# Kernel tuning notes

Measured on AMD Instinct MI355X. Metric: run time of the kernel, lower is better.

## Reference

```python
import jax, jax.numpy as jnp
import numpy as np

B, S, D, H = 2, 2048, 1024, 16
DK = D // H  # 64


def setup_inputs() -> dict:
    key = jax.random.key(0)
    ks = jax.random.split(key, 12)
    def lin(kw, kb, fan_in, shape_w):
        bound = 1.0 / np.sqrt(fan_in)
        W = jax.random.uniform(kw, shape_w, jnp.float32, -bound, bound)
        b = jax.random.uniform(kb, (shape_w[0],), jnp.float32, -bound, bound)
        return W, b
    Q = jax.random.normal(ks[0], (B, S, D), jnp.float32)
    K = jax.random.normal(ks[1], (B, S, D), jnp.float32)
    V = jax.random.normal(ks[2], (B, S, D), jnp.float32)
    attn_mask = jax.random.randint(ks[3], (B, S, S), 0, 2) == 1  # bool, True=masked
    Wq, bq = lin(ks[4], ks[5], D, (D, D))
    Wk, bk = lin(ks[6], ks[7], D, (D, D))
    Wv, bv = lin(ks[8], ks[9], D, (D, D))
    Wo, bo = lin(ks[10], ks[11], D, (D, D))
    return {"Q": Q, "K": K, "V": V, "attn_mask": attn_mask,
            "Wq": Wq, "bq": bq, "Wk": Wk, "bk": bk,
            "Wv": Wv, "bv": bv, "Wo": Wo, "bo": bo}


def reference(Q, K, V, attn_mask, Wq, bq, Wk, bk, Wv, bv, Wo, bo):
    b, s, d = Q.shape
    # project and split heads: [B,S,D] -> [B,H,S,DK]
    def heads(x, W, bias):
        y = x @ W.T + bias
        return y.reshape(b, -1, H, DK).transpose(0, 2, 1, 3)
    q = heads(Q, Wq, bq)
    k = heads(K, Wk, bk)
    v = heads(V, Wv, bv)
    # scaled dot-product attention with custom reweighting
    scores = jnp.einsum('bhqd,bhkd->bhqk', q, k) / np.sqrt(DK).astype(jnp.float32)
    scores = jnp.where(attn_mask[:, None, :, :], jnp.float32(-1e9), scores)
    attn_weights = jax.nn.softmax(scores, axis=-1) * scores.shape[-1]  # non-standard *S_k scale
    ctx = jnp.einsum('bhqk,bhkd->bhqd', attn_weights, v)
    ctx = ctx.transpose(0, 2, 1, 3).reshape(b, -1, H * DK)
    output = ctx @ Wo.T + bo
    return output, attn_weights
```

## Files before the change

kernel.cpp:

```cpp
#include <hip/hip_runtime.h>
#include <hip/hip_bf16.h>
#include <type_traits>

typedef __bf16 bf16_t;
typedef __attribute__((ext_vector_type(8))) __bf16 bf16x8;
typedef __attribute__((ext_vector_type(4))) float f32x4;

#define B_ 2
#define S_ 2048
#define D_ 1024
#define H_ 16
#define DK_ 64

__device__ inline void split8(const float* __restrict__ p, bf16x8& h, bf16x8& l) {
    float4 x0 = *(const float4*)p;
    float4 x1 = *(const float4*)(p + 4);
    float xs[8] = {x0.x, x0.y, x0.z, x0.w, x1.x, x1.y, x1.z, x1.w};
#pragma unroll
    for (int i = 0; i < 8; ++i) {
        bf16_t hh = (bf16_t)xs[i];
        h[i] = hh;
        l[i] = (bf16_t)(xs[i] - (float)hh);
    }
}
__device__ inline void hi8(const float* __restrict__ p, bf16x8& h) {
    float4 x0 = *(const float4*)p;
    float4 x1 = *(const float4*)(p + 4);
    float xs[8] = {x0.x, x0.y, x0.z, x0.w, x1.x, x1.y, x1.z, x1.w};
#pragma unroll
    for (int i = 0; i < 8; ++i) h[i] = (bf16_t)xs[i];
}

template <typename AT, typename OT, bool SPLIT>
__global__ __launch_bounds__(256) void gemm_bt(
    const AT* __restrict__ A,
    const float* __restrict__ W,
    const float* __restrict__ bias,
    OT* __restrict__ Y,
    int M, int N, int K)
{
    const int NB = N >> 6;
    const int bm = blockIdx.x / NB;
    const int bn = blockIdx.x % NB;
    const int tid  = threadIdx.x;
    const int wave = tid >> 6;
    const int lane = tid & 63;
    const int l16  = lane & 15;
    const int quad = lane >> 4;
    const int wm = wave >> 1, wn = wave & 1;

    __shared__ bf16_t Ah[64][40];
    __shared__ bf16_t Wh[64][40];
    __shared__ bf16_t Al[SPLIT ? 64 : 1][40];
    __shared__ bf16_t Wl[SPLIT ? 64 : 1][40];

    const int srow = tid >> 2;
    const int scol = (tid & 3) * 8;

    f32x4 acc[2][2];
#pragma unroll
    for (int i = 0; i < 2; ++i)
#pragma unroll
        for (int j = 0; j < 2; ++j) acc[i][j] = (f32x4){0.f, 0.f, 0.f, 0.f};

    const AT*    Arow = A + (size_t)(bm * 64 + srow) * K + scol;
    const float* Wrow = W + (size_t)(bn * 64 + srow) * K + scol;

    for (int k0 = 0; k0 < K; k0 += 32) {
        if constexpr (std::is_same_v<AT, float>) {
            bf16x8 ah, al;
            if constexpr (SPLIT) {
                split8(Arow + k0, ah, al);
                *(bf16x8*)(&Al[srow][scol]) = al;
            } else {
                hi8(Arow + k0, ah);
            }
            *(bf16x8*)(&Ah[srow][scol]) = ah;
        } else {
            *(bf16x8*)(&Ah[srow][scol]) = *(const bf16x8*)(Arow + k0);
        }
        {
            bf16x8 wh, wl;
            if constexpr (SPLIT) {
                split8(Wrow + k0, wh, wl);
                *(bf16x8*)(&Wl[srow][scol]) = wl;
            } else {
                hi8(Wrow + k0, wh);
            }
            *(bf16x8*)(&Wh[srow][scol]) = wh;
        }
        __syncthreads();

        bf16x8 afh[2], bfh[2], afl[2], bfl[2];
#pragma unroll
        for (int mi = 0; mi < 2; ++mi) {
            afh[mi] = *(const bf16x8*)(&Ah[wm * 32 + mi * 16 + l16][quad * 8]);
            if constexpr (SPLIT)
                afl[mi] = *(const bf16x8*)(&Al[wm * 32 + mi * 16 + l16][quad * 8]);
        }
#pragma unroll
        for (int ni = 0; ni < 2; ++ni) {
            bfh[ni] = *(const bf16x8*)(&Wh[wn * 32 + ni * 16 + l16][quad * 8]);
            if constexpr (SPLIT)
                bfl[ni] = *(const bf16x8*)(&Wl[wn * 32 + ni * 16 + l16][quad * 8]);
        }

#pragma unroll
        for (int mi = 0; mi < 2; ++mi)
#pragma unroll
            for (int ni = 0; ni < 2; ++ni) {
                acc[mi][ni] = __builtin_amdgcn_mfma_f32_16x16x32_bf16(
                    afh[mi], bfh[ni], acc[mi][ni], 0, 0, 0);
                if constexpr (SPLIT) {
                    acc[mi][ni] = __builtin_amdgcn_mfma_f32_16x16x32_bf16(
                        afl[mi], bfh[ni], acc[mi][ni], 0, 0, 0);
                    acc[mi][ni] = __builtin_amdgcn_mfma_f32_16x16x32_bf16(
                        afh[mi], bfl[ni], acc[mi][ni], 0, 0, 0);
                }
            }
        __syncthreads();
    }

#pragma unroll
    for (int ni = 0; ni < 2; ++ni) {
        const int col = bn * 64 + wn * 32 + ni * 16 + l16;
        const float bv = bias[col];
#pragma unroll
        for (int mi = 0; mi < 2; ++mi) {
#pragma unroll
            for (int r = 0; r < 4; ++r) {
                const int row = bm * 64 + wm * 32 + mi * 16 + quad * 4 + r;
                Y[(size_t)row * N + col] = (OT)(acc[mi][ni][r] + bv);
            }
        }
    }
}

__global__ __launch_bounds__(256) void pack_mask(
    const int* __restrict__ mask,
    unsigned long long* __restrict__ pk)
{
    const size_t nwords = (size_t)B_ * S_ * S_ / 64;
    const int lane = threadIdx.x & 63;
    size_t w = (size_t)blockIdx.x * 4 + (threadIdx.x >> 6);
    const size_t stride = (size_t)gridDim.x * 4;
    for (; w < nwords; w += stride) {
        const int m = mask[w * 64 + lane];
        const unsigned long long bb = __ballot(m != 0);
        if (lane == 0) pk[w] = bb;
    }
}

__global__ __launch_bounds__(256) void attn_kernel(
    const float*  __restrict__ qp,
    const float*  __restrict__ kp,
    const bf16_t* __restrict__ vp,
    const unsigned* __restrict__ pm,
    float* __restrict__ wout,
    float* __restrict__ normbuf,
    bf16_t* __restrict__ ctx)
{
    const int bid = blockIdx.x;
    const int qt = bid & 31;
    const int h  = (bid >> 5) & 15;
    const int b  = bid >> 9;
    const int tid  = threadIdx.x;
    const int wave = tid >> 6;
    const int lane = tid & 63;
    const int l16  = lane & 15;
    const int quad = lane >> 4;

    const int q0 = qt * 64 + wave * 16;

    __shared__ bf16_t Kh[32][72];
    __shared__ bf16_t Kl[32][72];
    __shared__ bf16_t vT[64][40];
    __shared__ bf16_t wl[4][16][40];

    const float* qbase = qp + ((size_t)(b * S_ + q0 + l16)) * D_ + h * DK_ + quad * 8;
    bf16x8 qh0, ql0, qh1, ql1;
    split8(qbase, qh0, ql0);
    split8(qbase + 32, qh1, ql1);

    const float scale = 0.125f;

    const int srow = tid >> 3;
    const int scol = (tid & 7) * 8;
    const float*  kst = kp + (size_t)b * S_ * D_ + h * DK_;
    const bf16_t* vst = vp + (size_t)b * S_ * D_ + h * DK_;

    const unsigned* pmrow = pm + (size_t)b * S_ * (S_ / 32);
    const size_t wbase = ((size_t)(b * H_ + h)) * S_ * S_;

    float lsum[4] = {0.f, 0.f, 0.f, 0.f};
    f32x4 acc[4];
#pragma unroll
    for (int t = 0; t < 4; ++t) acc[t] = (f32x4){0.f, 0.f, 0.f, 0.f};

    for (int j0 = 0; j0 < S_; j0 += 32) {
        {
            bf16x8 kh, kl;
            split8(kst + (size_t)(j0 + srow) * D_ + scol, kh, kl);
            *(bf16x8*)(&Kh[srow][scol]) = kh;
            *(bf16x8*)(&Kl[srow][scol]) = kl;

            const bf16x8 vv = *(const bf16x8*)(vst + (size_t)(j0 + srow) * D_ + scol);
#pragma unroll
            for (int i = 0; i < 8; ++i) vT[scol + i][srow] = vv[i];
        }
        unsigned mw[4];
#pragma unroll
        for (int r = 0; r < 4; ++r) {
            const int q = q0 + quad * 4 + r;
            mw[r] = pmrow[(size_t)q * (S_ / 32) + (j0 >> 5)];
        }
        __syncthreads();

#pragma unroll
        for (int sub = 0; sub < 2; ++sub) {
            const int rr = sub * 16 + l16;
            const bf16x8 kh0 = *(const bf16x8*)(&Kh[rr][quad * 8]);
            const bf16x8 kh1 = *(const bf16x8*)(&Kh[rr][32 + quad * 8]);
            const bf16x8 kl0 = *(const bf16x8*)(&Kl[rr][quad * 8]);
            const bf16x8 kl1 = *(const bf16x8*)(&Kl[rr][32 + quad * 8]);
            f32x4 c = (f32x4){0.f, 0.f, 0.f, 0.f};
            c = __builtin_amdgcn_mfma_f32_16x16x32_bf16(qh0, kh0, c, 0, 0, 0);
            c = __builtin_amdgcn_mfma_f32_16x16x32_bf16(qh1, kh1, c, 0, 0, 0);
            c = __builtin_amdgcn_mfma_f32_16x16x32_bf16(ql0, kh0, c, 0, 0, 0);
            c = __builtin_amdgcn_mfma_f32_16x16x32_bf16(ql1, kh1, c, 0, 0, 0);
            c = __builtin_amdgcn_mfma_f32_16x16x32_bf16(qh0, kl0, c, 0, 0, 0);
            c = __builtin_amdgcn_mfma_f32_16x16x32_bf16(qh1, kl1, c, 0, 0, 0);
            const int jt = j0 + sub * 16;
#pragma unroll
            for (int r = 0; r < 4; ++r) {
                const int q = q0 + quad * 4 + r;
                const int msk = (mw[r] >> (sub * 16 + l16)) & 1;
                const float e = msk ? 0.f : __expf(c[r] * scale);
                lsum[r] += e;
                __builtin_nontemporal_store(e, &wout[wbase + (size_t)q * S_ + jt + l16]);
                wl[wave][quad * 4 + r][sub * 16 + l16] = (bf16_t)e;
            }
        }
        const bf16x8 wa = *(const bf16x8*)(&wl[wave][l16][quad * 8]);
#pragma unroll
        for (int t = 0; t < 4; ++t) {
            const bf16x8 vf = *(const bf16x8*)(&vT[t * 16 + l16][quad * 8]);
            acc[t] = __builtin_amdgcn_mfma_f32_16x16x32_bf16(wa, vf, acc[t], 0, 0, 0);
        }
        __syncthreads();
    }

#pragma unroll
    for (int r = 0; r < 4; ++r) {
        float v = lsum[r];
        v += __shfl_xor(v, 1);
        v += __shfl_xor(v, 2);
        v += __shfl_xor(v, 4);
        v += __shfl_xor(v, 8);
        lsum[r] = v;
    }
    float norm[4];
#pragma unroll
    for (int r = 0; r < 4; ++r) norm[r] = 2048.f / lsum[r];

    if (l16 == 0) {
#pragma unroll
        for (int r = 0; r < 4; ++r)
            normbuf[(size_t)(b * H_ + h) * S_ + q0 + quad * 4 + r] = norm[r];
    }

#pragma unroll
    for (int t = 0; t < 4; ++t) {
#pragma unroll
        for (int r = 0; r < 4; ++r) {
            const int q = q0 + quad * 4 + r;
            ctx[((size_t)(b * S_ + q)) * D_ + h * DK_ + t * 16 + l16] =
                (bf16_t)(acc[t][r] * norm[r]);
        }
    }
}

__global__ __launch_bounds__(256) void rescale_wout(
    float* __restrict__ wout,
    const float* __restrict__ normbuf)
{
    const size_t total = (size_t)B_ * H_ * S_ * (S_ / 4);
    f32x4* wp = (f32x4*)wout;
    for (size_t i = (size_t)blockIdx.x * blockDim.x + threadIdx.x;
         i < total;
         i += (size_t)gridDim.x * blockDim.x) {
        const float n = normbuf[i >> 9];
        f32x4 w = __builtin_nontemporal_load(wp + i);
        w *= n;
        __builtin_nontemporal_store(w, wp + i);
    }
}

extern "C" void kernel_launch(void* const* d_in, const int* in_sizes, int n_in,
                              void* d_out, int out_size, void* d_ws, size_t ws_size,
                              hipStream_t stream) {
    const float* Q    = (const float*)d_in[0];
    const float* K    = (const float*)d_in[1];
    const float* V    = (const float*)d_in[2];
    const int*   mask = (const int*)d_in[3];
    const float* Wq   = (const float*)d_in[4];
    const float* bq   = (const float*)d_in[5];
    const float* Wk   = (const float*)d_in[6];
    const float* bk   = (const float*)d_in[7];
    const float* Wv   = (const float*)d_in[8];
    const float* bv   = (const float*)d_in[9];
    const float* Wo   = (const float*)d_in[10];
    const float* bo   = (const float*)d_in[11];

    const size_t BSD = (size_t)B_ * S_ * D_;
    float* out  = (float*)d_out;
    float* wout = out + BSD;

    float*  qp  = (float*)d_ws;
    float*  kpf = qp + BSD;
    bf16_t* vp  = (bf16_t*)(kpf + BSD);
    bf16_t* cx  = vp + BSD;
    unsigned long long* pk = (unsigned long long*)(cx + BSD);
    float* normbuf = (float*)((unsigned*)pk + (size_t)B_ * S_ * (S_ / 32));

    const int M = B_ * S_;
    const int N = D_;
    const int Kd = D_;
    const dim3 ggrid((M / 64) * (N / 64));
    const dim3 gblk(256);

    pack_mask<<<dim3(512), gblk, 0, stream>>>(mask, pk);

    gemm_bt<float, float, true><<<ggrid, gblk, 0, stream>>>(Q, Wq, bq, qp, M, N, Kd);
    gemm_bt<float, float, true><<<ggrid, gblk, 0, stream>>>(K, Wk, bk, kpf, M, N, Kd);
    gemm_bt<float, bf16_t, false><<<ggrid, gblk, 0, stream>>>(V, Wv, bv, vp, M, N, Kd);

    attn_kernel<<<dim3(B_ * H_ * (S_ / 64)), gblk, 0, stream>>>(
        qp, kpf, vp, (const unsigned*)pk, wout, normbuf, cx);

    gemm_bt<bf16_t, float, false><<<ggrid, gblk, 0, stream>>>(cx, Wo, bo, out, M, N, Kd);

    rescale_wout<<<dim3(2048), gblk, 0, stream>>>(wout, normbuf);
}
```

Measured before the change: 1.071 ms.

## Emit pre-split bf16 Q/K and head-transposed V from projection GEMMs

The projection GEMM epilogues now write Q and K as separate bf16 hi/lo planes, and V as bf16 in a per-head transposed [B,H,DK,S] layout. The attention kernel loads these directly instead of re-splitting fp32 K on every tile and transposing V element by element into shared memory. This cuts global read bytes for K and removes redundant conversion and scattered LDS writes in the hot loop. The cost is that the V epilogue now does strided scattered 2-byte global writes, and the Q/K GEMMs write two outputs each.

```diff
diff --git a/kernel.cpp b/kernel.cpp
--- a/kernel.cpp
+++ b/kernel.cpp
@@ -12,6 +12,8 @@
 #define H_ 16
 #define DK_ 64
 
+enum { OM_F32 = 0, OM_BF16 = 1, OM_SPLIT = 2, OM_HEADT = 3 };
+
 __device__ inline void split8(const float* __restrict__ p, bf16x8& h, bf16x8& l) {
     float4 x0 = *(const float4*)p;
     float4 x1 = *(const float4*)(p + 4);
@@ -31,12 +33,13 @@
     for (int i = 0; i < 8; ++i) h[i] = (bf16_t)xs[i];
 }
 
-template <typename AT, typename OT, bool SPLIT>
+template <typename AT, int OMODE, bool SPLIT>
 __global__ __launch_bounds__(256) void gemm_bt(
     const AT* __restrict__ A,
     const float* __restrict__ W,
     const float* __restrict__ bias,
-    OT* __restrict__ Y,
+    void* __restrict__ Yp,
+    void* __restrict__ Y2p,
     int M, int N, int K)
 {
     const int NB = N >> 6;
@@ -130,7 +133,23 @@
 #pragma unroll
             for (int r = 0; r < 4; ++r) {
                 const int row = bm * 64 + wm * 32 + mi * 16 + quad * 4 + r;
-                Y[(size_t)row * N + col] = (OT)(acc[mi][ni][r] + bv);
+                const float v = acc[mi][ni][r] + bv;
+                if constexpr (OMODE == OM_F32) {
+                    ((float*)Yp)[(size_t)row * N + col] = v;
+                } else if constexpr (OMODE == OM_BF16) {
+                    ((bf16_t*)Yp)[(size_t)row * N + col] = (bf16_t)v;
+                } else if constexpr (OMODE == OM_SPLIT) {
+                    const bf16_t hh = (bf16_t)v;
+                    ((bf16_t*)Yp)[(size_t)row * N + col] = hh;
+                    ((bf16_t*)Y2p)[(size_t)row * N + col] = (bf16_t)(v - (float)hh);
+                } else {
+                    const int bb  = row >> 11;
+                    const int ss  = row & (S_ - 1);
+                    const int hh2 = col >> 6;
+                    const int dk  = col & (DK_ - 1);
+                    ((bf16_t*)Yp)[((size_t)((bb * H_ + hh2) * DK_ + dk) << 11) + ss] =
+                        (bf16_t)v;
+                }
             }
         }
     }
@@ -152,9 +171,11 @@
 }
 
 __global__ __launch_bounds__(256) void attn_kernel(
-    const float*  __restrict__ qp,
-    const float*  __restrict__ kp,
-    const bf16_t* __restrict__ vp,
+    const bf16_t* __restrict__ qh_g,
+    const bf16_t* __restrict__ ql_g,
+    const bf16_t* __restrict__ kh_g,
+    const bf16_t* __restrict__ kl_g,
+    const bf16_t* __restrict__ vt_g,
     const unsigned* __restrict__ pm,
     float* __restrict__ wout,
     float* __restrict__ normbuf,
@@ -177,17 +198,21 @@
     __shared__ bf16_t vT[64][40];
     __shared__ bf16_t wl[4][16][40];
 
-    const float* qbase = qp + ((size_t)(b * S_ + q0 + l16)) * D_ + h * DK_ + quad * 8;
-    bf16x8 qh0, ql0, qh1, ql1;
-    split8(qbase, qh0, ql0);
-    split8(qbase + 32, qh1, ql1);
+    const size_t qoff = ((size_t)(b * S_ + q0 + l16)) * D_ + h * DK_ + quad * 8;
+    const bf16x8 qh0 = *(const bf16x8*)(qh_g + qoff);
+    const bf16x8 qh1 = *(const bf16x8*)(qh_g + qoff + 32);
+    const bf16x8 ql0 = *(const bf16x8*)(ql_g + qoff);
+    const bf16x8 ql1 = *(const bf16x8*)(ql_g + qoff + 32);
 
     const float scale = 0.125f;
 
-    const int srow = tid >> 3;
-    const int scol = (tid & 7) * 8;
-    const float*  kst = kp + (size_t)b * S_ * D_ + h * DK_;
-    const bf16_t* vst = vp + (size_t)b * S_ * D_ + h * DK_;
+    const int srow  = tid >> 3;
+    const int scol  = (tid & 7) * 8;
+    const int srow2 = tid >> 2;
+    const int scol2 = (tid & 3) * 8;
+    const bf16_t* khst = kh_g + (size_t)b * S_ * D_ + h * DK_;
+    const bf16_t* klst = kl_g + (size_t)b * S_ * D_ + h * DK_;
+    const bf16_t* vtst = vt_g + ((size_t)(b * H_ + h) * DK_ + srow2) * S_ + scol2;
 
     const unsigned* pmrow = pm + (size_t)b * S_ * (S_ / 32);
     const size_t wbase = ((size_t)(b * H_ + h)) * S_ * S_;
@@ -199,14 +224,10 @@
 
     for (int j0 = 0; j0 < S_; j0 += 32) {
         {
-            bf16x8 kh, kl;
-            split8(kst + (size_t)(j0 + srow) * D_ + scol, kh, kl);
-            *(bf16x8*)(&Kh[srow][scol]) = kh;
-            *(bf16x8*)(&Kl[srow][scol]) = kl;
-
-            const bf16x8 vv = *(const bf16x8*)(vst + (size_t)(j0 + srow) * D_ + scol);
-#pragma unroll
-            for (int i = 0; i < 8; ++i) vT[scol + i][srow] = vv[i];
+            const size_t ko = (size_t)(j0 + srow) * D_ + scol;
+            *(bf16x8*)(&Kh[srow][scol]) = *(const bf16x8*)(khst + ko);
+            *(bf16x8*)(&Kl[srow][scol]) = *(const bf16x8*)(klst + ko);
+            *(bf16x8*)(&vT[srow2][scol2]) = *(const bf16x8*)(vtst + j0);
         }
         unsigned mw[4];
 #pragma unroll
@@ -316,10 +337,12 @@
     float* out  = (float*)d_out;
     float* wout = out + BSD;
 
-    float*  qp  = (float*)d_ws;
-    float*  kpf = qp + BSD;
-    bf16_t* vp  = (bf16_t*)(kpf + BSD);
-    bf16_t* cx  = vp + BSD;
+    bf16_t* qh = (bf16_t*)d_ws;
+    bf16_t* ql = qh + BSD;
+    bf16_t* kh = ql + BSD;
+    bf16_t* kl = kh + BSD;
+    bf16_t* vt = kl + BSD;
+    bf16_t* cx = vt + BSD;
     unsigned long long* pk = (unsigned long long*)(cx + BSD);
     float* normbuf = (float*)((unsigned*)pk + (size_t)B_ * S_ * (S_ / 32));
 
@@ -331,14 +354,14 @@
 
     pack_mask<<<dim3(512), gblk, 0, stream>>>(mask, pk);
 
-    gemm_bt<float, float, true><<<ggrid, gblk, 0, stream>>>(Q, Wq, bq, qp, M, N, Kd);
-    gemm_bt<float, float, true><<<ggrid, gblk, 0, stream>>>(K, Wk, bk, kpf, M, N, Kd);
-    gemm_bt<float, bf16_t, false><<<ggrid, gblk, 0, stream>>>(V, Wv, bv, vp, M, N, Kd);
+    gemm_bt<float, OM_SPLIT, true><<<ggrid, gblk, 0, stream>>>(Q, Wq, bq, qh, ql, M, N, Kd);
+    gemm_bt<float, OM_SPLIT, true><<<ggrid, gblk, 0, stream>>>(K, Wk, bk, kh, kl, M, N, Kd);
+    gemm_bt<float, OM_HEADT, false><<<ggrid, gblk, 0, stream>>>(V, Wv, bv, vt, nullptr, M, N, Kd);
 
     attn_kernel<<<dim3(B_ * H_ * (S_ / 64)), gblk, 0, stream>>>(
-        qp, kpf, vp, (const unsigned*)pk, wout, normbuf, cx);
-
-    gemm_bt<bf16_t, float, false><<<ggrid, gblk, 0, stream>>>(cx, Wo, bo, out, M, N, Kd);
+        qh, ql, kh, kl, vt, (const unsigned*)pk, wout, normbuf, cx);
+
+    gemm_bt<bf16_t, OM_F32, false><<<ggrid, gblk, 0, stream>>>(cx, Wo, bo, out, nullptr, M, N, Kd);
 
     rescale_wout<<<dim3(2048), gblk, 0, stream>>>(wout, normbuf);
 }
```

New measurement: 1.065 ms. About the same (-0.6%).
